# Optimization experiments

Measured on AMD Instinct MI355X. Metric: run time of the kernel, lower is better.

Reference implementation:

```python
import jax, jax.numpy as jnp
import numpy as np

E = 768
H = 8

def setup_inputs() -> dict:
    key = jax.random.key(0)
    ks = jax.random.split(key, 9)
    s = 1.0 / np.sqrt(E)
    x = jax.random.normal(ks[0], (4, 2048, E), dtype=jnp.float32)
    Wq = jax.random.uniform(ks[1], (E, E), jnp.float32, -s, s)
    bq = jax.random.uniform(ks[2], (E,), jnp.float32, -s, s)
    Wk = jax.random.uniform(ks[3], (E, E), jnp.float32, -s, s)
    bk = jax.random.uniform(ks[4], (E,), jnp.float32, -s, s)
    Wv = jax.random.uniform(ks[5], (E, E), jnp.float32, -s, s)
    bv = jax.random.uniform(ks[6], (E,), jnp.float32, -s, s)
    Wo = jax.random.uniform(ks[7], (E, E), jnp.float32, -s, s)
    bo = jax.random.uniform(ks[8], (E,), jnp.float32, -s, s)
    return {"x": x, "Wq": Wq, "bq": bq, "Wk": Wk, "bk": bk, "Wv": Wv, "bv": bv, "Wo": Wo, "bo": bo}

def reference(x, Wq, bq, Wk, bk, Wv, bv, Wo, bo):
    B, N, Emb = x.shape
    d = Emb // H
    # projections (torch Linear: y = x @ W.T + b)
    q = (x @ Wq.T + bq).reshape(B, N, H, d).transpose(0, 2, 1, 3)  # [B,H,N,d]
    k = (x @ Wk.T + bk).reshape(B, N, H, d).transpose(0, 2, 1, 3)
    v = (x @ Wv.T + bv).reshape(B, N, H, d).transpose(0, 2, 1, 3)
    scores = jnp.einsum('bhnd,bhmd->bhnm', q, k) / jnp.sqrt(jnp.float32(d))
    attn = jax.nn.softmax(scores, axis=-1)  # dropout p=0.0 -> identity
    out = jnp.einsum('bhnm,bhmd->bhnd', attn, v)
    out = out.transpose(0, 2, 1, 3).reshape(B, N, Emb)
    return out @ Wo.T + bo
```

## Files before the change

### kernel.cpp

```cpp
#include <hip/hip_runtime.h>


#define E_DIM 768
#define N_HEAD 8
#define D_HEAD 96
#define B_SZ 4
#define N_SEQ 2048
#define BN (B_SZ * N_SEQ)

typedef unsigned short u16;
typedef __attribute__((ext_vector_type(8))) unsigned short u16x8;
typedef __attribute__((ext_vector_type(4))) unsigned short u16x4;
typedef __attribute__((ext_vector_type(8))) short s16x8;
typedef __attribute__((ext_vector_type(4))) float f32x4;

#define SZ_X   ((size_t)BN * E_DIM)
#define SZ_W   ((size_t)E_DIM * E_DIM)
#define SZ_B   ((size_t)E_DIM)
#define N_CONV (SZ_X + 4 * SZ_W + 4 * SZ_B)

__device__ __forceinline__ float bf2f(u16 u) {
    union { unsigned u; float f; } c; c.u = ((unsigned)u) << 16; return c.f;
}
__device__ __forceinline__ u16 f2bf(float f) {
    union { float f; unsigned u; } c; c.f = f;
    unsigned r = c.u + 0x7FFFu + ((c.u >> 16) & 1u);
    return (u16)(r >> 16);
}
__device__ __forceinline__ void gl_lds16(const u16* g, u16* l) {
    __builtin_amdgcn_global_load_lds(
        (const __attribute__((address_space(1))) unsigned int*)g,
        (__attribute__((address_space(3))) unsigned int*)l, 16, 0, 0);
}

__global__ void detect_dtype(const void* __restrict__ x, int* __restrict__ flag) {
    __shared__ int cnt;
    if (threadIdx.x == 0) cnt = 0;
    __syncthreads();
    const u16* p = (const u16*)x;
    u16 u = p[(size_t)threadIdx.x * 2];
    int ef = (u >> 7) & 0xFF;
    int insane = (ef < 96 || ef > 159) ? 1 : 0;
    atomicAdd(&cnt, insane);
    __syncthreads();
    if (threadIdx.x == 0) *flag = (cnt > 128) ? 1 : 0;
}

__global__ __launch_bounds__(256) void convert8(
    const int* __restrict__ flag,
    const void* __restrict__ x,
    const void* __restrict__ wq, const void* __restrict__ wk,
    const void* __restrict__ wv, const void* __restrict__ wo,
    const void* __restrict__ bq, const void* __restrict__ bk,
    const void* __restrict__ bv, const void* __restrict__ bo,
    u16* __restrict__ dst)
{
    size_t i = ((size_t)blockIdx.x * 256 + threadIdx.x) * 8;
    if (i >= N_CONV) return;
    const int f32 = *flag;
    size_t r = i;
    const void* s;
    if (r < SZ_X) { s = x; }
    else { r -= SZ_X;
      if (r < SZ_W) { s = wq; }
      else { r -= SZ_W;
        if (r < SZ_W) { s = wk; }
        else { r -= SZ_W;
          if (r < SZ_W) { s = wv; }
          else { r -= SZ_W;
            if (r < SZ_W) { s = wo; }
            else { r -= SZ_W;
              if (r < SZ_B) { s = bq; }
              else { r -= SZ_B;
                if (r < SZ_B) { s = bk; }
                else { r -= SZ_B;
                  if (r < SZ_B) { s = bv; }
                  else { r -= SZ_B; s = bo; }
                }
              }
            }
          }
        }
      }
    }
    u16x8 o;
    if (f32) {
        float4 a = ((const float4*)((const float*)s + r))[0];
        float4 b = ((const float4*)((const float*)s + r))[1];
        o[0] = f2bf(a.x); o[1] = f2bf(a.y); o[2] = f2bf(a.z); o[3] = f2bf(a.w);
        o[4] = f2bf(b.x); o[5] = f2bf(b.y); o[6] = f2bf(b.z); o[7] = f2bf(b.w);
    } else {
        o = *(const u16x8*)((const u16*)s + r);
    }
    *(u16x8*)(dst + i) = o;
}

#define GBK 64

#define GEMM_KLOOP(Ab, Wb)                                                           \
    for (int kt = 0; kt < E_DIM; kt += GBK) {                                        \
        __syncthreads();                                                             \
        _Pragma("unroll")                                                            \
        for (int j = 0; j < 4; j++) {                                                \
            int t = wave * 4 + j;                                                    \
            int row = t * 8 + (lane >> 3);                                           \
            int cl = (lane & 7) ^ ((lane >> 3) & 7);                                 \
            gl_lds16(Ab + (size_t)row * E_DIM + kt + cl * 8, &As[t * 8 * GBK]);      \
            gl_lds16(Wb + (size_t)row * E_DIM + kt + cl * 8, &Bs[t * 8 * GBK]);      \
        }                                                                            \
        __syncthreads();                                                             \
        _Pragma("unroll")                                                            \
        for (int s = 0; s < 2; s++) {                                                \
            s16x8 af[4], bf[4];                                                      \
            _Pragma("unroll")                                                        \
            for (int mi = 0; mi < 4; mi++) {                                         \
                int row = wm * 64 + mi * 16 + l16;                                   \
                af[mi] = *(const s16x8*)&As[row * GBK + ((s * 4 + q4) ^ (l16 & 7)) * 8]; \
            }                                                                        \
            _Pragma("unroll")                                                        \
            for (int ni = 0; ni < 4; ni++) {                                         \
                int row = wn * 64 + ni * 16 + l16;                                   \
                bf[ni] = *(const s16x8*)&Bs[row * GBK + ((s * 4 + q4) ^ (l16 & 7)) * 8]; \
            }                                                                        \
            _Pragma("unroll")                                                        \
            for (int mi = 0; mi < 4; mi++)                                           \
                _Pragma("unroll")                                                    \
                for (int ni = 0; ni < 4; ni++)                                       \
                    acc[mi][ni] = __builtin_amdgcn_mfma_f32_16x16x32_bf16(           \
                        af[mi], bf[ni], acc[mi][ni], 0, 0, 0);                       \
        }                                                                            \
    }

__global__ __launch_bounds__(256) void gemm_mfma_qkv(
    const u16* __restrict__ A, const u16* __restrict__ W,
    const u16* __restrict__ bias, u16* __restrict__ C, u16* __restrict__ Vt)
{
    __shared__ u16 smem[2 * 128 * GBK];
    u16* As = smem;
    u16* Bs = smem + 128 * GBK;
    const int tid = threadIdx.x;
    const int wave = tid >> 6, lane = tid & 63;
    const int q4 = lane >> 4, l16 = lane & 15;
    const int wm = wave & 1, wn = wave >> 1;
    const int bm = blockIdx.x, bn = blockIdx.y;

    f32x4 acc[4][4];
    #pragma unroll
    for (int i = 0; i < 4; i++)
        #pragma unroll
        for (int j = 0; j < 4; j++) acc[i][j] = (f32x4){0.f, 0.f, 0.f, 0.f};

    const u16* Ab = A + (size_t)(bm * 128) * E_DIM;
    const u16* Wb = W + (size_t)(bn * 128) * E_DIM;
    GEMM_KLOOP(Ab, Wb)

    if (bn < 12) {
        u16* Cb = smem;
        u16* Cw = C + (size_t)(bn / 6) * SZ_X;
        const int nc0 = (bn % 6) * 128;
        const int row = tid >> 3, seg = (tid & 7) * 16;
        #pragma unroll
        for (int mi = 0; mi < 4; mi++) {
            __syncthreads();
            #pragma unroll
            for (int ni = 0; ni < 4; ni++) {
                int n_l = wn * 64 + ni * 16 + l16;
                float bi = bf2f(bias[bn * 128 + n_l]);
                #pragma unroll
                for (int r = 0; r < 4; r++)
                    Cb[(wm * 16 + q4 * 4 + r) * 136 + n_l] = f2bf(acc[mi][ni][r] + bi);
            }
            __syncthreads();
            int mrow = bm * 128 + (row >> 4) * 64 + mi * 16 + (row & 15);
            *(u16x8*)(Cw + (size_t)mrow * E_DIM + nc0 + seg)     = *(const u16x8*)&Cb[row * 136 + seg];
            *(u16x8*)(Cw + (size_t)mrow * E_DIM + nc0 + seg + 8) = *(const u16x8*)&Cb[row * 136 + seg + 8];
        }
    } else {
        u16* Cb = smem;
        const int bnv = bn - 12;
        const int b = bm >> 4;
        const int n_l = tid >> 1, m0 = (tid & 1) * 16;
        const size_t vrow = (size_t)(b * 768 + bnv * 128 + n_l);
        #pragma unroll
        for (int mi = 0; mi < 4; mi++) {
            __syncthreads();
            #pragma unroll
            for (int ni = 0; ni < 4; ni++) {
                int nl = wn * 64 + ni * 16 + l16;
                float bi = bf2f(bias[bn * 128 + nl]);
                #pragma unroll
                for (int r = 0; r < 4; r++)
                    Cb[nl * 40 + wm * 16 + q4 * 4 + r] = f2bf(acc[mi][ni][r] + bi);
            }
            __syncthreads();
            int seq0 = (bm & 15) * 128 + (tid & 1) * 64 + mi * 16;
            *(u16x8*)(Vt + vrow * N_SEQ + seq0)     = *(const u16x8*)&Cb[n_l * 40 + m0];
            *(u16x8*)(Vt + vrow * N_SEQ + seq0 + 8) = *(const u16x8*)&Cb[n_l * 40 + m0 + 8];
        }
    }
}

__global__ __launch_bounds__(256) void gemm_mfma_out(
    const u16* __restrict__ A, const u16* __restrict__ W,
    const u16* __restrict__ bias, void* __restrict__ C,
    const int* __restrict__ flag)
{
    __shared__ u16 smem[2 * 128 * GBK];
    u16* As = smem;
    u16* Bs = smem + 128 * GBK;
    const int tid = threadIdx.x;
    const int wave = tid >> 6, lane = tid & 63;
    const int q4 = lane >> 4, l16 = lane & 15;
    const int wm = wave & 1, wn = wave >> 1;
    const int bm = blockIdx.x, bn = blockIdx.y;

    f32x4 acc[4][4];
    #pragma unroll
    for (int i = 0; i < 4; i++)
        #pragma unroll
        for (int j = 0; j < 4; j++) acc[i][j] = (f32x4){0.f, 0.f, 0.f, 0.f};

    const u16* Ab = A + (size_t)(bm * 128) * E_DIM;
    const u16* Wb = W + (size_t)(bn * 128) * E_DIM;
    GEMM_KLOOP(Ab, Wb)

    float* Cbf = (float*)smem;
    const int f32 = *flag;
    const int row = tid >> 3, seg = (tid & 7) * 16;
    #pragma unroll
    for (int mi = 0; mi < 4; mi++) {
        __syncthreads();
        #pragma unroll
        for (int ni = 0; ni < 4; ni++) {
            int n_l = wn * 64 + ni * 16 + l16;
            float bi = bf2f(bias[bn * 128 + n_l]);
            #pragma unroll
            for (int r = 0; r < 4; r++)
                Cbf[(wm * 16 + q4 * 4 + r) * 132 + n_l] = acc[mi][ni][r] + bi;
        }
        __syncthreads();
        int mrow = bm * 128 + (row >> 4) * 64 + mi * 16 + (row & 15);
        if (f32) {
            #pragma unroll
            for (int c = 0; c < 4; c++)
                *(float4*)((float*)C + (size_t)mrow * E_DIM + bn * 128 + seg + c * 4) =
                    *(const float4*)&Cbf[row * 132 + seg + c * 4];
        } else {
            u16x8 o0, o1;
            #pragma unroll
            for (int c = 0; c < 8; c++) {
                o0[c] = f2bf(Cbf[row * 132 + seg + c]);
                o1[c] = f2bf(Cbf[row * 132 + seg + 8 + c]);
            }
            *(u16x8*)((u16*)C + (size_t)mrow * E_DIM + bn * 128 + seg)     = o0;
            *(u16x8*)((u16*)C + (size_t)mrow * E_DIM + bn * 128 + seg + 8) = o1;
        }
    }
}

#define QT2 128
#define KT 64

__global__ __launch_bounds__(512) void attn_mfma2(
    const u16* __restrict__ Q, const u16* __restrict__ K,
    const u16* __restrict__ Vt, u16* __restrict__ O)
{
    __shared__ u16 Ks[3 * 64 * 32];
    __shared__ u16 Vts[2 * 96 * 32];
    __shared__ u16 Ps[8 * 16 * 72];

    const int tid = threadIdx.x;
    const int wave = tid >> 6, lane = tid & 63;
    const int q4 = lane >> 4, l16 = lane & 15;
    const int swz = (l16 >> 1) & 3;
    const int b = blockIdx.z, h = blockIdx.y, qb = blockIdx.x;

    const float SCL2 = 0.10206207261596577f * 1.4426950408889634f;

    const int qrow = qb * QT2 + wave * 16 + l16;
    const u16* qptr = Q + (size_t)(b * N_SEQ + qrow) * E_DIM + h * D_HEAD;
    s16x8 qf[3];
    #pragma unroll
    for (int ks = 0; ks < 3; ks++) {
        u16x8 raw = *(const u16x8*)(qptr + ks * 32 + q4 * 8);
        #pragma unroll
        for (int j = 0; j < 8; j++)
            qf[ks][j] = (short)f2bf(bf2f(raw[j]) * SCL2);
    }

    f32x4 of[6];
    #pragma unroll
    for (int i = 0; i < 6; i++) of[i] = (f32x4){0.f, 0.f, 0.f, 0.f};
    float l_r[4] = {0.f, 0.f, 0.f, 0.f};

    u16* psw = Ps + wave * 16 * 72;

    for (int kt = 0; kt < N_SEQ; kt += KT) {
        __syncthreads();
        #pragma unroll
        for (int ii = 0; ii < 3; ii++) {
            int t = wave + 8 * ii;
            if (t < 12) {
                int plane = t >> 2, sub = t & 3;
                int cip = sub * 64 + lane;
                int r = cip >> 2;
                int cs2 = (cip & 3) ^ ((r >> 1) & 3);
                gl_lds16(K + (size_t)(b * N_SEQ + kt + r) * E_DIM + h * D_HEAD + plane * 32 + cs2 * 8,
                         &Ks[plane * 2048 + sub * 512]);
            } else {
                int j = t - 12;
                int plane = j / 6, sub = j - plane * 6;
                int cip = sub * 64 + lane;
                int r = cip >> 2;
                int cs2 = (cip & 3) ^ ((r >> 1) & 3);
                gl_lds16(Vt + (size_t)((b * N_HEAD + h) * D_HEAD + r) * N_SEQ + kt + plane * 32 + cs2 * 8,
                         &Vts[plane * 3072 + sub * 512]);
            }
        }
        __syncthreads();

        f32x4 sf[4];
        #pragma unroll
        for (int i = 0; i < 4; i++) sf[i] = (f32x4){0.f, 0.f, 0.f, 0.f};
        #pragma unroll
        for (int nt = 0; nt < 4; nt++)
            #pragma unroll
            for (int ks = 0; ks < 3; ks++) {
                s16x8 bfr = *(const s16x8*)&Ks[ks * 2048 + (nt * 16 + l16) * 32 + ((q4 ^ swz) << 3)];
                sf[nt] = __builtin_amdgcn_mfma_f32_16x16x32_bf16(qf[ks], bfr, sf[nt], 0, 0, 0);
            }

        #pragma unroll
        for (int nt = 0; nt < 4; nt++)
            #pragma unroll
            for (int r = 0; r < 4; r++) {
                float pv = exp2f(sf[nt][r]);
                l_r[r] += pv;
                psw[(q4 * 4 + r) * 72 + nt * 16 + l16] = f2bf(pv);
            }

        #pragma unroll
        for (int ks2 = 0; ks2 < 2; ks2++) {
            s16x8 afr = *(const s16x8*)&psw[l16 * 72 + ks2 * 32 + q4 * 8];
            #pragma unroll
            for (int nt = 0; nt < 6; nt++) {
                s16x8 bfr = *(const s16x8*)&Vts[ks2 * 3072 + (nt * 16 + l16) * 32 + ((q4 ^ swz) << 3)];
                of[nt] = __builtin_amdgcn_mfma_f32_16x16x32_bf16(afr, bfr, of[nt], 0, 0, 0);
            }
        }
    }

    float linv[4];
    #pragma unroll
    for (int r = 0; r < 4; r++) {
        float l = l_r[r];
        #pragma unroll
        for (int off = 1; off < 16; off <<= 1)
            l += __shfl_xor(l, off, 64);
        linv[r] = 1.0f / l;
    }
    u16* optr = O + (size_t)(b * N_SEQ + qb * QT2 + wave * 16) * E_DIM + h * D_HEAD;
    #pragma unroll
    for (int nt = 0; nt < 6; nt++)
        #pragma unroll
        for (int r = 0; r < 4; r++)
            optr[(size_t)(q4 * 4 + r) * E_DIM + nt * 16 + l16] = f2bf(of[nt][r] * linv[r]);
}

extern "C" void kernel_launch(void* const* d_in, const int* in_sizes, int n_in,
                              void* d_out, int out_size, void* d_ws, size_t ws_size,
                              hipStream_t stream) {
    (void)in_sizes; (void)n_in; (void)out_size; (void)ws_size;
    const void* x  = d_in[0];
    const void* Wq = d_in[1]; const void* bq = d_in[2];
    const void* Wk = d_in[3]; const void* bk = d_in[4];
    const void* Wv = d_in[5]; const void* bv = d_in[6];
    const void* Wo = d_in[7]; const void* bo = d_in[8];

    int* flag = (int*)d_ws;
    u16* base = (u16*)d_ws + 8;
    u16* xb  = base;
    u16* wqb = xb  + SZ_X;
    u16* wob = wqb + 3 * SZ_W;
    u16* bqb = wob + SZ_W;
    u16* bob = bqb + 3 * SZ_B;
    u16* q_ws = bob + SZ_B;
    u16* k_ws = q_ws + SZ_X;
    u16* vt_ws = k_ws + SZ_X;
    u16* o_ws = vt_ws + SZ_X;

    detect_dtype<<<1, 256, 0, stream>>>(x, flag);
    convert8<<<(int)((N_CONV / 8 + 255) / 256), 256, 0, stream>>>(
        flag, x, Wq, Wk, Wv, Wo, bq, bk, bv, bo, base);

    gemm_mfma_qkv<<<dim3(BN / 128, 2304 / 128), 256, 0, stream>>>(
        xb, wqb, bqb, q_ws, vt_ws);

    attn_mfma2<<<dim3(N_SEQ / QT2, N_HEAD, B_SZ), 512, 0, stream>>>(
        q_ws, k_ws, vt_ws, o_ws);

    gemm_mfma_out<<<dim3(BN / 128, E_DIM / 128), 256, 0, stream>>>(
        o_ws, wob, bob, d_out, flag);
}
```

Before: 268.2 us.

## Double-buffer LDS tiles in GEMM and attention kernels, swizzle P buffer

Both projection GEMMs and the attention kernel now use two LDS buffers. Each iteration issues the async global-to-LDS loads for the next tile before computing on the current one, so each loop has one barrier instead of two and load latency is overlapped with MFMA work. The attention P scratch buffer drops its padded 72-element stride for a 64-element XOR-swizzled layout to avoid LDS bank conflicts in less space. The trade-off is doubled LDS for the K/V and GEMM tiles, which can lower the number of resident blocks per CU.

```diff
diff --git a/kernel.cpp b/kernel.cpp
--- a/kernel.cpp
+++ b/kernel.cpp
@@ -96,48 +96,62 @@
 }
 
 #define GBK 64
-
-#define GEMM_KLOOP(Ab, Wb)                                                           \
-    for (int kt = 0; kt < E_DIM; kt += GBK) {                                        \
-        __syncthreads();                                                             \
-        _Pragma("unroll")                                                            \
-        for (int j = 0; j < 4; j++) {                                                \
-            int t = wave * 4 + j;                                                    \
-            int row = t * 8 + (lane >> 3);                                           \
-            int cl = (lane & 7) ^ ((lane >> 3) & 7);                                 \
-            gl_lds16(Ab + (size_t)row * E_DIM + kt + cl * 8, &As[t * 8 * GBK]);      \
-            gl_lds16(Wb + (size_t)row * E_DIM + kt + cl * 8, &Bs[t * 8 * GBK]);      \
-        }                                                                            \
-        __syncthreads();                                                             \
-        _Pragma("unroll")                                                            \
-        for (int s = 0; s < 2; s++) {                                                \
-            s16x8 af[4], bf[4];                                                      \
-            _Pragma("unroll")                                                        \
-            for (int mi = 0; mi < 4; mi++) {                                         \
-                int row = wm * 64 + mi * 16 + l16;                                   \
-                af[mi] = *(const s16x8*)&As[row * GBK + ((s * 4 + q4) ^ (l16 & 7)) * 8]; \
-            }                                                                        \
-            _Pragma("unroll")                                                        \
-            for (int ni = 0; ni < 4; ni++) {                                         \
-                int row = wn * 64 + ni * 16 + l16;                                   \
-                bf[ni] = *(const s16x8*)&Bs[row * GBK + ((s * 4 + q4) ^ (l16 & 7)) * 8]; \
-            }                                                                        \
-            _Pragma("unroll")                                                        \
-            for (int mi = 0; mi < 4; mi++)                                           \
-                _Pragma("unroll")                                                    \
-                for (int ni = 0; ni < 4; ni++)                                       \
-                    acc[mi][ni] = __builtin_amdgcn_mfma_f32_16x16x32_bf16(           \
-                        af[mi], bf[ni], acc[mi][ni], 0, 0, 0);                       \
-        }                                                                            \
+#define GBUF (128 * GBK)
+
+#define GEMM_STAGE(Ab, Wb, kt, As_, Bs_)                                        \
+    {                                                                           \
+        const int kt_ = (kt);                                                   \
+        _Pragma("unroll")                                                       \
+        for (int j = 0; j < 4; j++) {                                           \
+            int st = wave * 4 + j;                                              \
+            int row = st * 8 + (lane >> 3);                                     \
+            int cl = (lane & 7) ^ ((lane >> 3) & 7);                            \
+            gl_lds16(Ab + (size_t)row * E_DIM + kt_ + cl * 8, (As_) + st * 512);\
+            gl_lds16(Wb + (size_t)row * E_DIM + kt_ + cl * 8, (Bs_) + st * 512);\
+        }                                                                       \
+    }
+
+#define GEMM_COMPUTE(As_, Bs_)                                                  \
+    {                                                                           \
+        _Pragma("unroll")                                                       \
+        for (int s = 0; s < 2; s++) {                                           \
+            s16x8 af[4], bf[4];                                                 \
+            _Pragma("unroll")                                                   \
+            for (int mi = 0; mi < 4; mi++) {                                    \
+                int row = wm * 64 + mi * 16 + l16;                              \
+                af[mi] = *(const s16x8*)&(As_)[row * GBK + ((s * 4 + q4) ^ (l16 & 7)) * 8]; \
+            }                                                                   \
+            _Pragma("unroll")                                                   \
+            for (int ni = 0; ni < 4; ni++) {                                    \
+                int row = wn * 64 + ni * 16 + l16;                              \
+                bf[ni] = *(const s16x8*)&(Bs_)[row * GBK + ((s * 4 + q4) ^ (l16 & 7)) * 8]; \
+            }                                                                   \
+            _Pragma("unroll")                                                   \
+            for (int mi = 0; mi < 4; mi++)                                      \
+                _Pragma("unroll")                                               \
+                for (int ni = 0; ni < 4; ni++)                                  \
+                    acc[mi][ni] = __builtin_amdgcn_mfma_f32_16x16x32_bf16(      \
+                        af[mi], bf[ni], acc[mi][ni], 0, 0, 0);                  \
+        }                                                                       \
+    }
+
+#define GEMM_KLOOP_DB(Ab, Wb)                                                   \
+    GEMM_STAGE(Ab, Wb, 0, smem, smem + GBUF)                                    \
+    for (int it = 0; it < 12; it++) {                                           \
+        __syncthreads();                                                        \
+        if (it < 11) {                                                          \
+            u16* An = smem + ((it + 1) & 1) * 2 * GBUF;                         \
+            GEMM_STAGE(Ab, Wb, (it + 1) * GBK, An, An + GBUF)                   \
+        }                                                                       \
+        u16* Ac = smem + (it & 1) * 2 * GBUF;                                   \
+        GEMM_COMPUTE(Ac, Ac + GBUF)                                             \
     }
 
 __global__ __launch_bounds__(256) void gemm_mfma_qkv(
     const u16* __restrict__ A, const u16* __restrict__ W,
     const u16* __restrict__ bias, u16* __restrict__ C, u16* __restrict__ Vt)
 {
-    __shared__ u16 smem[2 * 128 * GBK];
-    u16* As = smem;
-    u16* Bs = smem + 128 * GBK;
+    __shared__ u16 smem[4 * GBUF];
     const int tid = threadIdx.x;
     const int wave = tid >> 6, lane = tid & 63;
     const int q4 = lane >> 4, l16 = lane & 15;
@@ -152,7 +166,7 @@
 
     const u16* Ab = A + (size_t)(bm * 128) * E_DIM;
     const u16* Wb = W + (size_t)(bn * 128) * E_DIM;
-    GEMM_KLOOP(Ab, Wb)
+    GEMM_KLOOP_DB(Ab, Wb)
 
     if (bn < 12) {
         u16* Cb = smem;
@@ -205,9 +219,7 @@
     const u16* __restrict__ bias, void* __restrict__ C,
     const int* __restrict__ flag)
 {
-    __shared__ u16 smem[2 * 128 * GBK];
-    u16* As = smem;
-    u16* Bs = smem + 128 * GBK;
+    __shared__ u16 smem[4 * GBUF];
     const int tid = threadIdx.x;
     const int wave = tid >> 6, lane = tid & 63;
     const int q4 = lane >> 4, l16 = lane & 15;
@@ -222,7 +234,7 @@
 
     const u16* Ab = A + (size_t)(bm * 128) * E_DIM;
     const u16* Wb = W + (size_t)(bn * 128) * E_DIM;
-    GEMM_KLOOP(Ab, Wb)
+    GEMM_KLOOP_DB(Ab, Wb)
 
     float* Cbf = (float*)smem;
     const int f32 = *flag;
@@ -261,13 +273,38 @@
 #define QT2 128
 #define KT 64
 
+#define ATTN_STAGE(kt, bb)                                                       \
+    {                                                                            \
+        const int kt_ = (kt); const int bb_ = (bb);                              \
+        _Pragma("unroll")                                                        \
+        for (int ii = 0; ii < 3; ii++) {                                         \
+            int st = wave + 8 * ii;                                              \
+            if (st < 12) {                                                       \
+                int plane = st >> 2, sub = st & 3;                               \
+                int cip = sub * 64 + lane;                                       \
+                int r = cip >> 2;                                                \
+                int cs2 = (cip & 3) ^ ((r >> 1) & 3);                            \
+                gl_lds16(K + (size_t)(b * N_SEQ + kt_ + r) * E_DIM + h * D_HEAD + plane * 32 + cs2 * 8, \
+                         &Ks[bb_][plane * 2048 + sub * 512]);                    \
+            } else {                                                             \
+                int j = st - 12;                                                 \
+                int plane = j / 6, sub = j - plane * 6;                          \
+                int cip = sub * 64 + lane;                                       \
+                int r = cip >> 2;                                                \
+                int cs2 = (cip & 3) ^ ((r >> 1) & 3);                            \
+                gl_lds16(Vt + (size_t)((b * N_HEAD + h) * D_HEAD + r) * N_SEQ + kt_ + plane * 32 + cs2 * 8, \
+                         &Vts[bb_][plane * 3072 + sub * 512]);                   \
+            }                                                                    \
+        }                                                                        \
+    }
+
 __global__ __launch_bounds__(512) void attn_mfma2(
     const u16* __restrict__ Q, const u16* __restrict__ K,
     const u16* __restrict__ Vt, u16* __restrict__ O)
 {
-    __shared__ u16 Ks[3 * 64 * 32];
-    __shared__ u16 Vts[2 * 96 * 32];
-    __shared__ u16 Ps[8 * 16 * 72];
+    __shared__ u16 Ks[2][3 * 64 * 32];
+    __shared__ u16 Vts[2][2 * 96 * 32];
+    __shared__ u16 Ps[8 * 16 * 64];
 
     const int tid = threadIdx.x;
     const int wave = tid >> 6, lane = tid & 63;
@@ -293,31 +330,13 @@
     for (int i = 0; i < 6; i++) of[i] = (f32x4){0.f, 0.f, 0.f, 0.f};
     float l_r[4] = {0.f, 0.f, 0.f, 0.f};
 
-    u16* psw = Ps + wave * 16 * 72;
-
-    for (int kt = 0; kt < N_SEQ; kt += KT) {
+    u16* psw = Ps + wave * 16 * 64;
+
+    ATTN_STAGE(0, 0)
+    for (int t = 0; t < N_SEQ / KT; t++) {
         __syncthreads();
-        #pragma unroll
-        for (int ii = 0; ii < 3; ii++) {
-            int t = wave + 8 * ii;
-            if (t < 12) {
-                int plane = t >> 2, sub = t & 3;
-                int cip = sub * 64 + lane;
-                int r = cip >> 2;
-                int cs2 = (cip & 3) ^ ((r >> 1) & 3);
-                gl_lds16(K + (size_t)(b * N_SEQ + kt + r) * E_DIM + h * D_HEAD + plane * 32 + cs2 * 8,
-                         &Ks[plane * 2048 + sub * 512]);
-            } else {
-                int j = t - 12;
-                int plane = j / 6, sub = j - plane * 6;
-                int cip = sub * 64 + lane;
-                int r = cip >> 2;
-                int cs2 = (cip & 3) ^ ((r >> 1) & 3);
-                gl_lds16(Vt + (size_t)((b * N_HEAD + h) * D_HEAD + r) * N_SEQ + kt + plane * 32 + cs2 * 8,
-                         &Vts[plane * 3072 + sub * 512]);
-            }
-        }
-        __syncthreads();
+        if (t < N_SEQ / KT - 1) ATTN_STAGE((t + 1) * KT, (t + 1) & 1)
+        const int cb = t & 1;
 
         f32x4 sf[4];
         #pragma unroll
@@ -326,7 +345,7 @@
         for (int nt = 0; nt < 4; nt++)
             #pragma unroll
             for (int ks = 0; ks < 3; ks++) {
-                s16x8 bfr = *(const s16x8*)&Ks[ks * 2048 + (nt * 16 + l16) * 32 + ((q4 ^ swz) << 3)];
+                s16x8 bfr = *(const s16x8*)&Ks[cb][ks * 2048 + (nt * 16 + l16) * 32 + ((q4 ^ swz) << 3)];
                 sf[nt] = __builtin_amdgcn_mfma_f32_16x16x32_bf16(qf[ks], bfr, sf[nt], 0, 0, 0);
             }
 
@@ -336,15 +355,16 @@
             for (int r = 0; r < 4; r++) {
                 float pv = exp2f(sf[nt][r]);
                 l_r[r] += pv;
-                psw[(q4 * 4 + r) * 72 + nt * 16 + l16] = f2bf(pv);
+                int prow = q4 * 4 + r;
+                psw[prow * 64 + (((nt * 2 + (l16 >> 3)) ^ (prow & 7)) << 3) + (l16 & 7)] = f2bf(pv);
             }
 
         #pragma unroll
         for (int ks2 = 0; ks2 < 2; ks2++) {
-            s16x8 afr = *(const s16x8*)&psw[l16 * 72 + ks2 * 32 + q4 * 8];
+            s16x8 afr = *(const s16x8*)&psw[l16 * 64 + (((ks2 * 4 + q4) ^ (l16 & 7)) << 3)];
             #pragma unroll
             for (int nt = 0; nt < 6; nt++) {
-                s16x8 bfr = *(const s16x8*)&Vts[ks2 * 3072 + (nt * 16 + l16) * 32 + ((q4 ^ swz) << 3)];
+                s16x8 bfr = *(const s16x8*)&Vts[cb][ks2 * 3072 + (nt * 16 + l16) * 32 + ((q4 ^ swz) << 3)];
                 of[nt] = __builtin_amdgcn_mfma_f32_16x16x32_bf16(afr, bfr, of[nt], 0, 0, 0);
             }
         }
```

New measurement: 245.1 us. 8.6% less time.
